# Optimization experiments

Hardware: AMD Instinct MI355X
Metric: run time of the kernel (lower is better)

The kernel has to match this reference:

```python
import jax, jax.numpy as jnp
import numpy as np

N_NODES = 100000
N_EDGES = 1600000
NIN = 128
NHID = 128
N_GRAPHS = 1024


def _gcn_conv(x, src, dst, norm, W, b, n_nodes):
    """PyG-style GCNConv: linear (no bias) -> normalized scatter-add -> + bias."""
    xw = x @ W                                   # [N, out]
    msg = xw[src] * norm[:, None]                # gather + edge-normalize, [E', out]
    out = jax.ops.segment_sum(msg, dst, num_segments=n_nodes)
    return out + b


def _gcn_norm(edge_index, n_nodes):
    """Add self-loops and compute symmetric deg^{-1/2} normalization per edge."""
    loops = jnp.arange(n_nodes, dtype=edge_index.dtype)
    src = jnp.concatenate([edge_index[0], loops])
    dst = jnp.concatenate([edge_index[1], loops])
    deg = jax.ops.segment_sum(jnp.ones_like(dst, dtype=jnp.float32), dst,
                              num_segments=n_nodes)
    deg_isqrt = jnp.where(deg > 0, jax.lax.rsqrt(jnp.maximum(deg, 1.0)), 0.0)
    norm = deg_isqrt[src] * deg_isqrt[dst]
    return src, dst, norm


def setup_inputs() -> dict:
    key = jax.random.key(0)
    ks = jax.random.split(key, 8)
    x = jax.random.normal(ks[0], (N_NODES, NIN), dtype=jnp.float32)
    edge_index = jax.random.randint(ks[1], (2, N_EDGES), 0, N_NODES, dtype=jnp.int64)
    batch = jnp.sort(jax.random.randint(ks[2], (N_NODES,), 0, N_GRAPHS, dtype=jnp.int64))
    s_in = 1.0 / np.sqrt(NIN)
    s_h = 1.0 / np.sqrt(NHID)
    return {
        "x": x,
        "edge_index": edge_index,
        "batch": batch,
        "W1": jax.random.normal(ks[3], (NIN, NHID), dtype=jnp.float32) * s_in,
        "b1": jnp.zeros((NHID,), dtype=jnp.float32),
        "W2": jax.random.normal(ks[4], (NHID, NHID), dtype=jnp.float32) * s_h,
        "b2": jnp.zeros((NHID,), dtype=jnp.float32),
        "W3": jax.random.normal(ks[5], (NHID, NHID), dtype=jnp.float32) * s_h,
        "b3": jnp.zeros((NHID,), dtype=jnp.float32),
        "Wfc": jax.random.normal(ks[6], (NHID, 1), dtype=jnp.float32) * s_h,
        "bfc": jnp.zeros((1,), dtype=jnp.float32),
    }


def reference(x, edge_index, batch, W1, b1, W2, b2, W3, b3, Wfc, bfc):
    n_nodes = x.shape[0]
    src, dst, norm = _gcn_norm(edge_index, n_nodes)
    h = jax.nn.relu(_gcn_conv(x, src, dst, norm, W1, b1, n_nodes))
    h = jax.nn.relu(_gcn_conv(h, src, dst, norm, W2, b2, n_nodes))
    h = jax.nn.relu(_gcn_conv(h, src, dst, norm, W3, b3, n_nodes))
    # global mean pool over graphs in the batch
    sums = jax.ops.segment_sum(h, batch, num_segments=N_GRAPHS)      # [G, NHID]
    cnts = jax.ops.segment_sum(jnp.ones((n_nodes,), dtype=h.dtype), batch,
                               num_segments=N_GRAPHS)
    pooled = sums / jnp.maximum(cnts, 1.0)[:, None]
    return pooled @ Wfc + bfc                                        # [G, 1]
```

## Files before the change

kernel.cpp:

```cpp
#include <hip/hip_runtime.h>

#define N_NODES   100000
#define N_EDGES   1600000
#define NFEAT     128
#define N_GRAPHS  1024

#define BSHIFT  8
#define BNODES  256
#define NBUCK   391
#define BCAP    4608
#define SC_EDGES 4096
#define SC_EPT   8
#define SC_BLOCKS 391
#define BD_EPT   18

#define WT_STRIDE 136
#define GEMM_BLOCKS 782

typedef unsigned int uint32;
typedef unsigned short ushort;
typedef __attribute__((ext_vector_type(8))) short short8;
typedef __attribute__((ext_vector_type(4))) float f32x4;

__device__ inline ushort f2b(float f) {
    uint32 x = __float_as_uint(f);
    uint32 r = x + 0x7fffu + ((x >> 16) & 1u);
    return (ushort)(r >> 16);
}
__device__ inline float blo(uint32 u) { return __uint_as_float(u << 16); }
__device__ inline float bhi(uint32 u) { return __uint_as_float(u & 0xffff0000u); }

__device__ inline short8 cvt8(const float* p) {
    float4 v0 = ((const float4*)p)[0];
    float4 v1 = ((const float4*)p)[1];
    short8 r;
    r[0] = (short)f2b(v0.x); r[1] = (short)f2b(v0.y);
    r[2] = (short)f2b(v0.z); r[3] = (short)f2b(v0.w);
    r[4] = (short)f2b(v1.x); r[5] = (short)f2b(v1.y);
    r[6] = (short)f2b(v1.z); r[7] = (short)f2b(v1.w);
    return r;
}

__global__ __launch_bounds__(256) void k_castw(const float* __restrict__ W1, const float* __restrict__ W2,
                                               const float* __restrict__ W3, ushort* __restrict__ WT,
                                               int* __restrict__ cur) {
    int i = blockIdx.x * blockDim.x + threadIdx.x;
    if (i < NBUCK) cur[i] = 0;
    if (i >= 3 * NFEAT * NFEAT) return;
    int l = i >> 14;
    int j = i & 16383;
    int n = j >> 7;
    int k = j & 127;
    const float* W = (l == 0) ? W1 : (l == 1) ? W2 : W3;
    WT[i] = f2b(W[k * NFEAT + n]);
}

struct SMemScatter {
    int hist[NBUCK], lofs[NBUCK], gbase[NBUCK];
    int wsum[4];
    uint32 sortedP[SC_EDGES];
    ushort sortedB[SC_EDGES];
};

__global__ __launch_bounds__(512) void k_phase1(const int* __restrict__ src, const int* __restrict__ dst,
                                                int* __restrict__ cur, uint32* __restrict__ bbuf,
                                                const float* __restrict__ A, const ushort* __restrict__ WTl,
                                                ushort* __restrict__ C, int M) {
    __shared__ __align__(16) char smem[NFEAT * WT_STRIDE * 2];
    int t = threadIdx.x;
    if (blockIdx.x < SC_BLOCKS) {
        SMemScatter& S = *(SMemScatter*)smem;
        int e0 = blockIdx.x * SC_EDGES;
        int total = N_EDGES - e0; if (total > SC_EDGES) total = SC_EDGES; if (total < 0) total = 0;
        for (int i = t; i < NBUCK; i += 512) S.hist[i] = 0;
        __syncthreads();
        uint32 val[SC_EPT];
        int    meta[SC_EPT];
        #pragma unroll
        for (int k = 0; k < SC_EPT; ++k) {
            int i = t + k * 512;
            meta[k] = -1;
            if (i < total) {
                int s = src[e0 + i], d = dst[e0 + i];
                int b = d >> BSHIFT;
                int tk = atomicAdd(&S.hist[b], 1);
                val[k] = ((uint32)(d & (BNODES - 1)) << 17) | (uint32)s;
                meta[k] = (b << 13) | tk;
            }
        }
        __syncthreads();
        int inc = 0, ts = 0, h0 = 0;
        if (t < 256) {
            int b0 = 2 * t, b1 = 2 * t + 1;
            h0 = (b0 < NBUCK) ? S.hist[b0] : 0;
            int h1 = (b1 < NBUCK) ? S.hist[b1] : 0;
            ts = h0 + h1;
            int lane = t & 63;
            inc = ts;
            #pragma unroll
            for (int d = 1; d < 64; d <<= 1) {
                int u = __shfl_up(inc, d, 64);
                if (lane >= d) inc += u;
            }
            if (lane == 63) S.wsum[t >> 6] = inc;
        }
        __syncthreads();
        if (t < 256) {
            int w = t >> 6;
            int wpre = 0;
            for (int i = 0; i < w; ++i) wpre += S.wsum[i];
            int run = wpre + inc - ts;
            int b0 = 2 * t, b1 = 2 * t + 1;
            int h1 = ts - h0;
            if (b0 < NBUCK) {
                S.lofs[b0] = run;
                if (h0) S.gbase[b0] = atomicAdd(&cur[b0], h0);
            }
            if (b1 < NBUCK) {
                S.lofs[b1] = run + h0;
                if (h1) S.gbase[b1] = atomicAdd(&cur[b1], h1);
            }
        }
        __syncthreads();
        #pragma unroll
        for (int k = 0; k < SC_EPT; ++k) {
            if (meta[k] >= 0) {
                int b = meta[k] >> 13;
                int p = S.lofs[b] + (meta[k] & 0x1FFF);
                S.sortedP[p] = val[k];
                S.sortedB[p] = (ushort)b;
            }
        }
        __syncthreads();
        for (int i = t; i < total; i += 512) {
            int b = S.sortedB[i];
            int addr = S.gbase[b] + (i - S.lofs[b]);
            if (addr < BCAP)
                bbuf[(size_t)b * BCAP + addr] = S.sortedP[i];
        }
    } else {
        ushort* sWT = (ushort*)smem;
        int gb = blockIdx.x - SC_BLOCKS;
        for (int i = t; i < NFEAT * 16; i += 512) {
            int n = i >> 4, c = i & 15;
            *(float4*)(sWT + n * WT_STRIDE + c * 8) = ((const float4*)WTl)[i];
        }
        int wave = t >> 6, lane = t & 63;
        int m0 = gb * 128 + wave * 16;
        int mRow = m0 + (lane & 15);
        if (mRow >= M) mRow = M - 1;
        int kg = lane >> 4;
        const float* Ap = A + (size_t)mRow * NFEAT + kg * 8;
        short8 a0 = cvt8(Ap);
        short8 a1 = cvt8(Ap + 32);
        short8 a2 = cvt8(Ap + 64);
        short8 a3 = cvt8(Ap + 96);
        __syncthreads();

        f32x4 acc[8];
        #pragma unroll
        for (int nt = 0; nt < 8; ++nt) acc[nt] = (f32x4){0.f, 0.f, 0.f, 0.f};
        #pragma unroll
        for (int nt = 0; nt < 8; ++nt) {
            int n = nt * 16 + (lane & 15);
            const short8* Bp = (const short8*)(sWT + n * WT_STRIDE + kg * 8);
            short8 b0 = Bp[0];
            short8 b1 = Bp[4];
            short8 b2 = Bp[8];
            short8 b3 = Bp[12];
            acc[nt] = __builtin_amdgcn_mfma_f32_16x16x32_bf16(a0, b0, acc[nt], 0, 0, 0);
            acc[nt] = __builtin_amdgcn_mfma_f32_16x16x32_bf16(a1, b1, acc[nt], 0, 0, 0);
            acc[nt] = __builtin_amdgcn_mfma_f32_16x16x32_bf16(a2, b2, acc[nt], 0, 0, 0);
            acc[nt] = __builtin_amdgcn_mfma_f32_16x16x32_bf16(a3, b3, acc[nt], 0, 0, 0);
        }
        __syncthreads();
        {
            int colBase = lane & 15;
            #pragma unroll
            for (int r = 0; r < 4; ++r) {
                int lr = wave * 16 + kg * 4 + r;
                #pragma unroll
                for (int nt = 0; nt < 8; ++nt)
                    sWT[lr * NFEAT + nt * 16 + colBase] = f2b(acc[nt][r]);
            }
        }
        __syncthreads();
        {
            int rowBase = gb * 128;
            const float4* sC4 = (const float4*)sWT;
            for (int i = t; i < 2048; i += 512) {
                int row = i >> 4;
                int gr = rowBase + row;
                if (gr < M) ((float4*)(C + (size_t)gr * NFEAT))[i & 15] = sC4[i];
            }
        }
    }
}

__global__ __launch_bounds__(256) void k_build(const uint32* __restrict__ bbuf, const int* __restrict__ cur,
                                               int* __restrict__ col, int* __restrict__ offsets,
                                               float* __restrict__ dinv) {
    int b = blockIdx.x;
    __shared__ int hist[BNODES], excl[BNODES];
    __shared__ int wsum[4], wtot[4];
    __shared__ int sorted[BCAP];
    __shared__ int sBase, sTotal;
    int t = threadIdx.x;
    {
        int pre = 0, tot = 0;
        #pragma unroll
        for (int q = 0; q < 2; ++q) {
            int i = 2 * t + q;
            if (i < NBUCK) {
                int v = cur[i]; if (v > BCAP) v = BCAP;
                tot += v;
                if (i < b) pre += v;
            }
        }
        int lane = t & 63, w = t >> 6;
        #pragma unroll
        for (int d = 32; d > 0; d >>= 1) { pre += __shfl_down(pre, d, 64); tot += __shfl_down(tot, d, 64); }
        if (lane == 0) { wsum[w] = pre; wtot[w] = tot; }
        __syncthreads();
        if (t == 0) {
            sBase = wsum[0] + wsum[1] + wsum[2] + wsum[3];
            sTotal = wtot[0] + wtot[1] + wtot[2] + wtot[3];
        }
        hist[t] = 0;
    }
    __syncthreads();
    int base = sBase;
    if (b == NBUCK - 1 && t == 0) offsets[N_NODES] = sTotal;
    int cnt = cur[b]; if (cnt > BCAP) cnt = BCAP;
    const uint32* reg = bbuf + (size_t)b * BCAP;

    uint32 val[BD_EPT];
    int    meta[BD_EPT];
    #pragma unroll
    for (int k = 0; k < BD_EPT; ++k) {
        int i = t + k * 256;
        meta[k] = -1;
        if (i < cnt) {
            uint32 p = reg[i];
            int node = p >> 17;
            int tk = atomicAdd(&hist[node], 1);
            val[k] = p & 0x1FFFF;
            meta[k] = (node << 16) | tk;
        }
    }
    __syncthreads();
    {
        int c = hist[t];
        int lane = t & 63, w = t >> 6;
        int inc = c;
        #pragma unroll
        for (int d = 1; d < 64; d <<= 1) {
            int u = __shfl_up(inc, d, 64);
            if (lane >= d) inc += u;
        }
        if (lane == 63) wsum[w] = inc;
        __syncthreads();
        int wpre = 0;
        for (int i = 0; i < w; ++i) wpre += wsum[i];
        int e = wpre + inc - c;
        excl[t] = e;
        int node = (b << BSHIFT) + t;
        if (node < N_NODES) {
            offsets[node] = base + e;
            dinv[node] = rsqrtf((float)(c + 1));
        }
    }
    __syncthreads();
    #pragma unroll
    for (int k = 0; k < BD_EPT; ++k) {
        if (meta[k] >= 0) {
            int node = meta[k] >> 16;
            sorted[excl[node] + (meta[k] & 0xFFFF)] = (int)val[k];
        }
    }
    __syncthreads();
    for (int i = t; i < cnt; i += 256) col[base + i] = sorted[i];
}

__global__ __launch_bounds__(512) void k_gemm(const ushort* __restrict__ A,
                                              const ushort* __restrict__ WTl,
                                              ushort* __restrict__ C, int M) {
    __shared__ ushort sWT[NFEAT * WT_STRIDE];
    int t = threadIdx.x;
    for (int i = t; i < NFEAT * 16; i += 512) {
        int n = i >> 4, c = i & 15;
        *(float4*)(sWT + n * WT_STRIDE + c * 8) = ((const float4*)WTl)[i];
    }
    int wave = t >> 6, lane = t & 63;
    int m0 = blockIdx.x * 128 + wave * 16;
    int mRow = m0 + (lane & 15);
    if (mRow >= M) mRow = M - 1;
    int kg = lane >> 4;
    const short8* Ap = (const short8*)(A + (size_t)mRow * NFEAT + kg * 8);
    short8 a0 = Ap[0];
    short8 a1 = Ap[4];
    short8 a2 = Ap[8];
    short8 a3 = Ap[12];
    __syncthreads();

    f32x4 acc[8];
    #pragma unroll
    for (int nt = 0; nt < 8; ++nt) acc[nt] = (f32x4){0.f, 0.f, 0.f, 0.f};
    #pragma unroll
    for (int nt = 0; nt < 8; ++nt) {
        int n = nt * 16 + (lane & 15);
        const short8* Bp = (const short8*)(sWT + n * WT_STRIDE + kg * 8);
        short8 b0 = Bp[0];
        short8 b1 = Bp[4];
        short8 b2 = Bp[8];
        short8 b3 = Bp[12];
        acc[nt] = __builtin_amdgcn_mfma_f32_16x16x32_bf16(a0, b0, acc[nt], 0, 0, 0);
        acc[nt] = __builtin_amdgcn_mfma_f32_16x16x32_bf16(a1, b1, acc[nt], 0, 0, 0);
        acc[nt] = __builtin_amdgcn_mfma_f32_16x16x32_bf16(a2, b2, acc[nt], 0, 0, 0);
        acc[nt] = __builtin_amdgcn_mfma_f32_16x16x32_bf16(a3, b3, acc[nt], 0, 0, 0);
    }
    __syncthreads();
    {
        int colBase = lane & 15;
        #pragma unroll
        for (int r = 0; r < 4; ++r) {
            int lr = wave * 16 + kg * 4 + r;
            #pragma unroll
            for (int nt = 0; nt < 8; ++nt)
                sWT[lr * NFEAT + nt * 16 + colBase] = f2b(acc[nt][r]);
        }
    }
    __syncthreads();
    {
        int rowBase = blockIdx.x * 128;
        const float4* sC4 = (const float4*)sWT;
        for (int i = t; i < 2048; i += 512) {
            int row = i >> 4;
            int gr = rowBase + row;
            if (gr < M) ((float4*)(C + (size_t)gr * NFEAT))[i & 15] = sC4[i];
        }
    }
}

#define AGG_GROUP4 \
    int half = lane >> 4; \
    int fl = lane & 15; \
    float dn = dinv[n]; \
    int e0 = off[n], e1 = off[n + 1]; \
    int deg = e1 - e0; \
    int maxd = deg; \
    { int u16 = __shfl_xor(maxd, 16, 64); if (u16 > maxd) maxd = u16; \
      int u32 = __shfl_xor(maxd, 32, 64); if (u32 > maxd) maxd = u32; } \
    const uint4* XW4 = (const uint4*)XWu; \
    uint4 sv = XW4[(size_t)n * 16 + fl]; \
    float ws = dn * dn; \
    float a0 = ws * blo(sv.x), a1 = ws * bhi(sv.x); \
    float a2 = ws * blo(sv.y), a3 = ws * bhi(sv.y); \
    float a4 = ws * blo(sv.z), a5 = ws * bhi(sv.z); \
    float a6 = ws * blo(sv.w), a7 = ws * bhi(sv.w); \
    int cm = 0; float wm = 0.f; \
    if (fl < deg) { cm = col[e0 + fl]; wm = dn * dinv[cm]; } \
    for (int base = 0; base < maxd; base += 16) { \
        int nb = base + 16; \
        int cmn = 0; float wmn = 0.f; \
        if (nb + fl < deg) { cmn = col[e0 + nb + fl]; wmn = dn * dinv[cmn]; } \
        int lim = maxd - base; if (lim > 16) lim = 16; \
        for (int j = 0; j < lim; j += 8) { \
            uint4 u[8]; float w[8]; \
            _Pragma("unroll") \
            for (int p = 0; p < 8; ++p) { \
                int sl = (half << 4) + j + p; \
                int cc = __shfl(cm, sl, 64); \
                w[p] = __shfl(wm, sl, 64); \
                u[p] = XW4[(size_t)cc * 16 + fl]; \
            } \
            _Pragma("unroll") \
            for (int p = 0; p < 8; ++p) { \
                a0 = fmaf(w[p], blo(u[p].x), a0); a1 = fmaf(w[p], bhi(u[p].x), a1); \
                a2 = fmaf(w[p], blo(u[p].y), a2); a3 = fmaf(w[p], bhi(u[p].y), a3); \
                a4 = fmaf(w[p], blo(u[p].z), a4); a5 = fmaf(w[p], bhi(u[p].z), a5); \
                a6 = fmaf(w[p], blo(u[p].w), a6); a7 = fmaf(w[p], bhi(u[p].w), a7); \
            } \
        } \
        cm = cmn; wm = wmn; \
    }

__global__ __launch_bounds__(256) void k_agg(const uint32* __restrict__ XWu, const int* __restrict__ col,
                                             const int* __restrict__ off, const float* __restrict__ dinv,
                                             const float* __restrict__ bias, uint32* __restrict__ Hu) {
    int wid = (blockIdx.x * blockDim.x + threadIdx.x) >> 6;
    int lane = threadIdx.x & 63;
    int n = (wid << 2) + (lane >> 4);
    if (n >= N_NODES) return;
    AGG_GROUP4
    float4 bb0 = ((const float4*)bias)[2 * fl];
    float4 bb1 = ((const float4*)bias)[2 * fl + 1];
    float r0 = fmaxf(a0 + bb0.x, 0.f), r1 = fmaxf(a1 + bb0.y, 0.f);
    float r2 = fmaxf(a2 + bb0.z, 0.f), r3 = fmaxf(a3 + bb0.w, 0.f);
    float r4 = fmaxf(a4 + bb1.x, 0.f), r5 = fmaxf(a5 + bb1.y, 0.f);
    float r6 = fmaxf(a6 + bb1.z, 0.f), r7 = fmaxf(a7 + bb1.w, 0.f);
    uint4 o;
    o.x = (uint32)f2b(r0) | ((uint32)f2b(r1) << 16);
    o.y = (uint32)f2b(r2) | ((uint32)f2b(r3) << 16);
    o.z = (uint32)f2b(r4) | ((uint32)f2b(r5) << 16);
    o.w = (uint32)f2b(r6) | ((uint32)f2b(r7) << 16);
    ((uint4*)Hu)[(size_t)n * 16 + fl] = o;
}

__global__ __launch_bounds__(256) void k_agg_fc(const uint32* __restrict__ XWu, const int* __restrict__ col,
                                                const int* __restrict__ off, const float* __restrict__ dinv,
                                                const float* __restrict__ bias, const float* __restrict__ Wfc,
                                                float* __restrict__ nodeS) {
    int wid = (blockIdx.x * blockDim.x + threadIdx.x) >> 6;
    int lane = threadIdx.x & 63;
    int n = (wid << 2) + (lane >> 4);
    if (n >= N_NODES) return;
    AGG_GROUP4
    float4 bb0 = ((const float4*)bias)[2 * fl];
    float4 bb1 = ((const float4*)bias)[2 * fl + 1];
    float4 wf0 = ((const float4*)Wfc)[2 * fl];
    float4 wf1 = ((const float4*)Wfc)[2 * fl + 1];
    float s = fmaxf(a0 + bb0.x, 0.f) * wf0.x + fmaxf(a1 + bb0.y, 0.f) * wf0.y
            + fmaxf(a2 + bb0.z, 0.f) * wf0.z + fmaxf(a3 + bb0.w, 0.f) * wf0.w
            + fmaxf(a4 + bb1.x, 0.f) * wf1.x + fmaxf(a5 + bb1.y, 0.f) * wf1.y
            + fmaxf(a6 + bb1.z, 0.f) * wf1.z + fmaxf(a7 + bb1.w, 0.f) * wf1.w;
    s += __shfl_xor(s, 8, 64);
    s += __shfl_xor(s, 4, 64);
    s += __shfl_xor(s, 2, 64);
    s += __shfl_xor(s, 1, 64);
    if (fl == 0) nodeS[n] = s;
}

__device__ inline int lower_bound_dev(const int* a, int n, int key) {
    int lo = 0, hi = n;
    while (lo < hi) {
        int mid = (lo + hi) >> 1;
        if (a[mid] < key) lo = mid + 1; else hi = mid;
    }
    return lo;
}

__global__ __launch_bounds__(256) void k_pool(const float* __restrict__ nodeS, const int* __restrict__ batch,
                                              const float* __restrict__ bfc, float* __restrict__ out) {
    int g = blockIdx.x;
    int t = threadIdx.x;
    int lo = lower_bound_dev(batch, N_NODES, g);
    int hi = lower_bound_dev(batch, N_NODES, g + 1);
    float s = 0.f;
    for (int i = lo + t; i < hi; i += 256) s += nodeS[i];
    for (int d = 32; d > 0; d >>= 1) s += __shfl_down(s, d, 64);
    __shared__ float ws[4];
    int lane = t & 63, w = t >> 6;
    if (lane == 0) ws[w] = s;
    __syncthreads();
    if (t == 0) {
        float tot = ws[0] + ws[1] + ws[2] + ws[3];
        float cnt = (float)(hi - lo);
        out[g] = tot / fmaxf(cnt, 1.0f) + bfc[0];
    }
}

extern "C" void kernel_launch(void* const* d_in, const int* in_sizes, int n_in,
                              void* d_out, int out_size, void* d_ws, size_t ws_size,
                              hipStream_t stream) {
    const float* x    = (const float*)d_in[0];
    const int*   ei   = (const int*)d_in[1];
    const int*   batch= (const int*)d_in[2];
    const float* W1   = (const float*)d_in[3];
    const float* b1   = (const float*)d_in[4];
    const float* W2   = (const float*)d_in[5];
    const float* b2   = (const float*)d_in[6];
    const float* W3   = (const float*)d_in[7];
    const float* b3   = (const float*)d_in[8];
    const float* Wfc  = (const float*)d_in[9];
    const float* bfc  = (const float*)d_in[10];
    float* out = (float*)d_out;

    const int* src = ei;
    const int* dst = ei + N_EDGES;

    char* p = (char*)d_ws;
    auto carve = [&](size_t bytes) { void* r = (void*)p; p += (bytes + 255) & ~(size_t)255; return r; };
    int*    cur       = (int*)   carve(sizeof(int) * NBUCK);
    uint32* bbuf      = (uint32*)carve(sizeof(uint32) * (size_t)NBUCK * BCAP);
    float*  dinv      = (float*) carve(sizeof(float) * N_NODES);
    int*    offsets   = (int*)   carve(sizeof(int) * (N_NODES + 1));
    int*    col       = (int*)   carve(sizeof(int) * N_EDGES);
    ushort* XW        = (ushort*)carve(sizeof(short) * (size_t)N_NODES * NFEAT);
    ushort* H         = (ushort*)carve(sizeof(short) * (size_t)N_NODES * NFEAT);
    ushort* WT        = (ushort*)carve(sizeof(short) * 3 * NFEAT * NFEAT);
    float*  nodeS     = (float*) carve(sizeof(float) * N_NODES);

    const int aggBlocks = (N_NODES + 15) / 16;

    k_castw<<<(3 * NFEAT * NFEAT + 255) / 256, 256, 0, stream>>>(W1, W2, W3, WT, cur);
    k_phase1<<<SC_BLOCKS + GEMM_BLOCKS, 512, 0, stream>>>(src, dst, cur, bbuf, x, WT, XW, N_NODES);
    k_build<<<NBUCK, 256, 0, stream>>>(bbuf, cur, col, offsets, dinv);

    k_agg<<<aggBlocks, 256, 0, stream>>>((const uint32*)XW, col, offsets, dinv, b1, (uint32*)H);
    k_gemm<<<GEMM_BLOCKS, 512, 0, stream>>>(H, WT + NFEAT * NFEAT, XW, N_NODES);
    k_agg<<<aggBlocks, 256, 0, stream>>>((const uint32*)XW, col, offsets, dinv, b2, (uint32*)H);
    k_gemm<<<GEMM_BLOCKS, 512, 0, stream>>>(H, WT + 2 * NFEAT * NFEAT, XW, N_NODES);
    k_agg_fc<<<aggBlocks, 256, 0, stream>>>((const uint32*)XW, col, offsets, dinv, b3, Wfc, nodeS);

    k_pool<<<N_GRAPHS, 256, 0, stream>>>(nodeS, batch, bfc, out);
}
```

Before: 354.2 us.

## Fuse aggregation with the following layer's GEMM into one kernel

Merges the per-node aggregation (bias, ReLU, bf16 pack) with the next layer's 128x128 MFMA GEMM. Each 256-thread block aggregates 16 nodes into shared memory, then its 4 waves each compute two 16-column tiles and write XW for the next layer directly. This removes the H round trip through global memory and two kernel launches. In exchange, each wave reads its W tile from global/L2 instead of shared memory, and the block now has extra barriers on the gather-bound path. The block count drops the ceil, which relies on N_NODES being divisible by 16.

```diff
diff --git a/kernel.cpp b/kernel.cpp
--- a/kernel.cpp
+++ b/kernel.cpp
@@ -280,66 +280,6 @@
     }
     __syncthreads();
     for (int i = t; i < cnt; i += 256) col[base + i] = sorted[i];
-}
-
-__global__ __launch_bounds__(512) void k_gemm(const ushort* __restrict__ A,
-                                              const ushort* __restrict__ WTl,
-                                              ushort* __restrict__ C, int M) {
-    __shared__ ushort sWT[NFEAT * WT_STRIDE];
-    int t = threadIdx.x;
-    for (int i = t; i < NFEAT * 16; i += 512) {
-        int n = i >> 4, c = i & 15;
-        *(float4*)(sWT + n * WT_STRIDE + c * 8) = ((const float4*)WTl)[i];
-    }
-    int wave = t >> 6, lane = t & 63;
-    int m0 = blockIdx.x * 128 + wave * 16;
-    int mRow = m0 + (lane & 15);
-    if (mRow >= M) mRow = M - 1;
-    int kg = lane >> 4;
-    const short8* Ap = (const short8*)(A + (size_t)mRow * NFEAT + kg * 8);
-    short8 a0 = Ap[0];
-    short8 a1 = Ap[4];
-    short8 a2 = Ap[8];
-    short8 a3 = Ap[12];
-    __syncthreads();
-
-    f32x4 acc[8];
-    #pragma unroll
-    for (int nt = 0; nt < 8; ++nt) acc[nt] = (f32x4){0.f, 0.f, 0.f, 0.f};
-    #pragma unroll
-    for (int nt = 0; nt < 8; ++nt) {
-        int n = nt * 16 + (lane & 15);
-        const short8* Bp = (const short8*)(sWT + n * WT_STRIDE + kg * 8);
-        short8 b0 = Bp[0];
-        short8 b1 = Bp[4];
-        short8 b2 = Bp[8];
-        short8 b3 = Bp[12];
-        acc[nt] = __builtin_amdgcn_mfma_f32_16x16x32_bf16(a0, b0, acc[nt], 0, 0, 0);
-        acc[nt] = __builtin_amdgcn_mfma_f32_16x16x32_bf16(a1, b1, acc[nt], 0, 0, 0);
-        acc[nt] = __builtin_amdgcn_mfma_f32_16x16x32_bf16(a2, b2, acc[nt], 0, 0, 0);
-        acc[nt] = __builtin_amdgcn_mfma_f32_16x16x32_bf16(a3, b3, acc[nt], 0, 0, 0);
-    }
-    __syncthreads();
-    {
-        int colBase = lane & 15;
-        #pragma unroll
-        for (int r = 0; r < 4; ++r) {
-            int lr = wave * 16 + kg * 4 + r;
-            #pragma unroll
-            for (int nt = 0; nt < 8; ++nt)
-                sWT[lr * NFEAT + nt * 16 + colBase] = f2b(acc[nt][r]);
-        }
-    }
-    __syncthreads();
-    {
-        int rowBase = blockIdx.x * 128;
-        const float4* sC4 = (const float4*)sWT;
-        for (int i = t; i < 2048; i += 512) {
-            int row = i >> 4;
-            int gr = rowBase + row;
-            if (gr < M) ((float4*)(C + (size_t)gr * NFEAT))[i & 15] = sC4[i];
-        }
-    }
 }
 
 #define AGG_GROUP4 \
@@ -385,26 +325,72 @@
         cm = cmn; wm = wmn; \
     }
 
-__global__ __launch_bounds__(256) void k_agg(const uint32* __restrict__ XWu, const int* __restrict__ col,
-                                             const int* __restrict__ off, const float* __restrict__ dinv,
-                                             const float* __restrict__ bias, uint32* __restrict__ Hu) {
-    int wid = (blockIdx.x * blockDim.x + threadIdx.x) >> 6;
-    int lane = threadIdx.x & 63;
-    int n = (wid << 2) + (lane >> 4);
-    if (n >= N_NODES) return;
+__global__ __launch_bounds__(256) void k_agg_gemm(const uint32* __restrict__ XWu,
+                                                  const int* __restrict__ col,
+                                                  const int* __restrict__ off,
+                                                  const float* __restrict__ dinv,
+                                                  const float* __restrict__ bias,
+                                                  const ushort* __restrict__ WTl,
+                                                  ushort* __restrict__ C) {
+    __shared__ __align__(16) ushort sA[16 * WT_STRIDE];
+    int t = threadIdx.x;
+    int lane = t & 63;
+    int lw = t >> 6;
+    int n = (blockIdx.x << 4) + (lw << 2) + (lane >> 4);
     AGG_GROUP4
-    float4 bb0 = ((const float4*)bias)[2 * fl];
-    float4 bb1 = ((const float4*)bias)[2 * fl + 1];
-    float r0 = fmaxf(a0 + bb0.x, 0.f), r1 = fmaxf(a1 + bb0.y, 0.f);
-    float r2 = fmaxf(a2 + bb0.z, 0.f), r3 = fmaxf(a3 + bb0.w, 0.f);
-    float r4 = fmaxf(a4 + bb1.x, 0.f), r5 = fmaxf(a5 + bb1.y, 0.f);
-    float r6 = fmaxf(a6 + bb1.z, 0.f), r7 = fmaxf(a7 + bb1.w, 0.f);
-    uint4 o;
-    o.x = (uint32)f2b(r0) | ((uint32)f2b(r1) << 16);
-    o.y = (uint32)f2b(r2) | ((uint32)f2b(r3) << 16);
-    o.z = (uint32)f2b(r4) | ((uint32)f2b(r5) << 16);
-    o.w = (uint32)f2b(r6) | ((uint32)f2b(r7) << 16);
-    ((uint4*)Hu)[(size_t)n * 16 + fl] = o;
+    {
+        float4 bb0 = ((const float4*)bias)[2 * fl];
+        float4 bb1 = ((const float4*)bias)[2 * fl + 1];
+        float r0 = fmaxf(a0 + bb0.x, 0.f), r1 = fmaxf(a1 + bb0.y, 0.f);
+        float r2 = fmaxf(a2 + bb0.z, 0.f), r3 = fmaxf(a3 + bb0.w, 0.f);
+        float r4 = fmaxf(a4 + bb1.x, 0.f), r5 = fmaxf(a5 + bb1.y, 0.f);
+        float r6 = fmaxf(a6 + bb1.z, 0.f), r7 = fmaxf(a7 + bb1.w, 0.f);
+        uint4 o;
+        o.x = (uint32)f2b(r0) | ((uint32)f2b(r1) << 16);
+        o.y = (uint32)f2b(r2) | ((uint32)f2b(r3) << 16);
+        o.z = (uint32)f2b(r4) | ((uint32)f2b(r5) << 16);
+        o.w = (uint32)f2b(r6) | ((uint32)f2b(r7) << 16);
+        int lrow = (lw << 2) + half;
+        *(uint4*)(sA + lrow * WT_STRIDE + fl * 8) = o;
+    }
+    __syncthreads();
+    {
+        const short8* Ap = (const short8*)(sA + fl * WT_STRIDE + half * 8);
+        short8 af0 = Ap[0];
+        short8 af1 = Ap[4];
+        short8 af2 = Ap[8];
+        short8 af3 = Ap[12];
+        f32x4 acc[2];
+        acc[0] = (f32x4){0.f, 0.f, 0.f, 0.f};
+        acc[1] = (f32x4){0.f, 0.f, 0.f, 0.f};
+        #pragma unroll
+        for (int q = 0; q < 2; ++q) {
+            int nt = lw * 2 + q;
+            const short8* Bp = (const short8*)(WTl + (nt * 16 + fl) * NFEAT + half * 8);
+            short8 b0 = Bp[0];
+            short8 b1 = Bp[4];
+            short8 b2 = Bp[8];
+            short8 b3 = Bp[12];
+            acc[q] = __builtin_amdgcn_mfma_f32_16x16x32_bf16(af0, b0, acc[q], 0, 0, 0);
+            acc[q] = __builtin_amdgcn_mfma_f32_16x16x32_bf16(af1, b1, acc[q], 0, 0, 0);
+            acc[q] = __builtin_amdgcn_mfma_f32_16x16x32_bf16(af2, b2, acc[q], 0, 0, 0);
+            acc[q] = __builtin_amdgcn_mfma_f32_16x16x32_bf16(af3, b3, acc[q], 0, 0, 0);
+        }
+        __syncthreads();
+        #pragma unroll
+        for (int q = 0; q < 2; ++q) {
+            int nt = lw * 2 + q;
+            #pragma unroll
+            for (int r = 0; r < 4; ++r)
+                sA[(half * 4 + r) * NFEAT + nt * 16 + fl] = f2b(acc[q][r]);
+        }
+    }
+    __syncthreads();
+    {
+        int row = t >> 4;
+        float4 v = ((const float4*)sA)[t];
+        ((float4*)(C + (size_t)((blockIdx.x << 4) + row) * NFEAT))[t & 15] = v;
+    }
 }
 
 __global__ __launch_bounds__(256) void k_agg_fc(const uint32* __restrict__ XWu, const int* __restrict__ col,
@@ -487,20 +473,20 @@
     int*    offsets   = (int*)   carve(sizeof(int) * (N_NODES + 1));
     int*    col       = (int*)   carve(sizeof(int) * N_EDGES);
     ushort* XW        = (ushort*)carve(sizeof(short) * (size_t)N_NODES * NFEAT);
-    ushort* H         = (ushort*)carve(sizeof(short) * (size_t)N_NODES * NFEAT);
+    ushort* XW2       = (ushort*)carve(sizeof(short) * (size_t)N_NODES * NFEAT);
     ushort* WT        = (ushort*)carve(sizeof(short) * 3 * NFEAT * NFEAT);
     float*  nodeS     = (float*) carve(sizeof(float) * N_NODES);
 
-    const int aggBlocks = (N_NODES + 15) / 16;
+    const int aggBlocks = N_NODES / 16;
 
     k_castw<<<(3 * NFEAT * NFEAT + 255) / 256, 256, 0, stream>>>(W1, W2, W3, WT, cur);
     k_phase1<<<SC_BLOCKS + GEMM_BLOCKS, 512, 0, stream>>>(src, dst, cur, bbuf, x, WT, XW, N_NODES);
     k_build<<<NBUCK, 256, 0, stream>>>(bbuf, cur, col, offsets, dinv);
 
-    k_agg<<<aggBlocks, 256, 0, stream>>>((const uint32*)XW, col, offsets, dinv, b1, (uint32*)H);
-    k_gemm<<<GEMM_BLOCKS, 512, 0, stream>>>(H, WT + NFEAT * NFEAT, XW, N_NODES);
-    k_agg<<<aggBlocks, 256, 0, stream>>>((const uint32*)XW, col, offsets, dinv, b2, (uint32*)H);
-    k_gemm<<<GEMM_BLOCKS, 512, 0, stream>>>(H, WT + 2 * NFEAT * NFEAT, XW, N_NODES);
+    k_agg_gemm<<<aggBlocks, 256, 0, stream>>>((const uint32*)XW, col, offsets, dinv, b1,
+                                              WT + NFEAT * NFEAT, XW2);
+    k_agg_gemm<<<aggBlocks, 256, 0, stream>>>((const uint32*)XW2, col, offsets, dinv, b2,
+                                              WT + 2 * NFEAT * NFEAT, XW);
     k_agg_fc<<<aggBlocks, 256, 0, stream>>>((const uint32*)XW, col, offsets, dinv, b3, Wfc, nodeS);
 
     k_pool<<<N_GRAPHS, 256, 0, stream>>>(nodeS, batch, bfc, out);
```

Result: no change. 351.4 us (-0.8%).
